# Performance work log

Measured on AMD Instinct MI355X. Metric: run time of the kernel, lower is better.

Reference implementation:

```python
import jax, jax.numpy as jnp
import numpy as np

BLOCK_K = 128  # per_1x128 block quantization: block_n=1 (per row), block_k=128


def _dequant(wq, scale):
    # wq: [E, N, K] quantized codes; scale: [E, N, ceil(K/BLOCK_K)]
    K = wq.shape[-1]
    s_full = jnp.repeat(scale, BLOCK_K, axis=-1)[..., :K]
    return wq * s_full


def setup_inputs() -> dict:
    key = jax.random.key(0)
    ks = jax.random.split(key, 6)
    T, E, H, I = 1024, 8, 1024, 768
    x = jax.random.normal(ks[0], (T, H), dtype=jnp.float32)
    router_logits = jax.random.normal(ks[1], (T, E), dtype=jnp.float32)
    # fp8 codes simulated as float values; block scales positive (scale_inv)
    w13_weight = jax.random.normal(ks[2], (E, 2 * I, H), dtype=jnp.float32) * 0.05
    w13_weight_scale_inv = jax.random.uniform(ks[3], (E, 2 * I, H // BLOCK_K), dtype=jnp.float32, minval=0.5, maxval=1.5)
    w2_weight = jax.random.normal(ks[4], (E, H, I), dtype=jnp.float32) * 0.05
    w2_weight_scale_inv = jax.random.uniform(ks[5], (E, H, I // BLOCK_K), dtype=jnp.float32, minval=0.5, maxval=1.5)
    return {
        "x": x,
        "router_logits": router_logits,
        "w13_weight": w13_weight,
        "w13_weight_scale_inv": w13_weight_scale_inv,
        "w2_weight": w2_weight,
        "w2_weight_scale_inv": w2_weight_scale_inv,
        "top_k": 2,
    }


def reference(x, router_logits, w13_weight, w13_weight_scale_inv, w2_weight, w2_weight_scale_inv, top_k):
    T, H = x.shape
    E = router_logits.shape[-1]
    I = w2_weight.shape[-1]

    # ---- dequantize block-scaled weights (inline dequant of fp8 grouped GEMM) ----
    w13 = _dequant(w13_weight, w13_weight_scale_inv)   # [E, 2I, H]
    w2 = _dequant(w2_weight, w2_weight_scale_inv)      # [E, H, I]

    # ---- routing: softmax scoring, top_k, renormalize ----
    probs = jax.nn.softmax(router_logits, axis=-1)     # [T, E]
    topk_w, topk_idx = jax.lax.top_k(probs, top_k)     # [T, K]
    topk_w = topk_w / jnp.sum(topk_w, axis=-1, keepdims=True)  # renormalize=True
    # dense combine weights [T, E] (scatter of top_k routing weights)
    combine = jnp.zeros((T, E), x.dtype).at[jnp.arange(T)[:, None], topk_idx].add(topk_w)

    # ---- grouped expert FFN (dense-over-experts reference) ----
    gate_up = jnp.einsum('th,enh->ten', x, w13)        # [T, E, 2I]
    gate, up = gate_up[..., :I], gate_up[..., I:]
    act = jax.nn.silu(gate) * up                       # silu activation ('silu')
    out_e = jnp.einsum('tei,ehi->teh', act, w2)        # [T, E, H]

    # ---- combine ----
    return jnp.einsum('teh,te->th', out_e, combine)    # [T, H]
```

## Files before the change

### kernel.cpp

```cpp
#include <hip/hip_runtime.h>

#define T_TOK 1024
#define H_DIM 1024
#define I_DIM 768
#define E_NUM 8

#define G13 1572864
#define G2   786432
#define GX   131072
#define PREP_BLOCKS 10240

typedef __bf16 bf16x8 __attribute__((ext_vector_type(8)));
typedef float  f32x4  __attribute__((ext_vector_type(4)));

__device__ inline bf16x8 cvt8(float4 a, float4 b, float s) {
    bf16x8 o;
    o[0] = (__bf16)(a.x * s); o[1] = (__bf16)(a.y * s);
    o[2] = (__bf16)(a.z * s); o[3] = (__bf16)(a.w * s);
    o[4] = (__bf16)(b.x * s); o[5] = (__bf16)(b.y * s);
    o[6] = (__bf16)(b.z * s); o[7] = (__bf16)(b.w * s);
    return o;
}

__global__ __launch_bounds__(256) void prep_kernel(
    const float* __restrict__ w13, const float* __restrict__ w13s,
    const float* __restrict__ w2,  const float* __restrict__ w2s,
    const float* __restrict__ x,   float4* __restrict__ out4,
    __bf16* __restrict__ w13d, __bf16* __restrict__ w2d, __bf16* __restrict__ xbf,
    const float* __restrict__ logits,
    int* __restrict__ counts, int* __restrict__ base,
    int* __restrict__ tok_list, float* __restrict__ wt_list)
{
    if (blockIdx.x == PREP_BLOCKS) {
        __shared__ int cnt[E_NUM];
        const int t0 = threadIdx.x;
        if (t0 < E_NUM) cnt[t0] = 0;
        __syncthreads();
#pragma unroll
        for (int tt = 0; tt < 4; tt++) {
            int t = t0 + tt * 256;
            float l[E_NUM];
#pragma unroll
            for (int e = 0; e < E_NUM; e++) l[e] = logits[t * E_NUM + e];
            int e0 = 0; float m0 = l[0];
#pragma unroll
            for (int e = 1; e < E_NUM; e++) if (l[e] > m0) { m0 = l[e]; e0 = e; }
            int e1 = -1; float m1 = -3e38f;
#pragma unroll
            for (int e = 0; e < E_NUM; e++) if (e != e0 && l[e] > m1) { m1 = l[e]; e1 = e; }
            float w0 = 1.0f / (1.0f + expf(m1 - m0));
            float w1 = 1.0f - w0;
            int p0 = atomicAdd(&cnt[e0], 1);
            tok_list[e0 * T_TOK + p0] = t;
            wt_list[e0 * T_TOK + p0] = w0;
            int p1 = atomicAdd(&cnt[e1], 1);
            tok_list[e1 * T_TOK + p1] = t;
            wt_list[e1 * T_TOK + p1] = w1;
        }
        __syncthreads();
        if (t0 == 0) {
            int s = 0;
            for (int e = 0; e < E_NUM; e++) { base[e] = s; counts[e] = cnt[e]; s += cnt[e]; }
        }
        return;
    }

    int g = blockIdx.x * 256 + threadIdx.x;
    if (g < G13) {
        int k8 = g & 127;
        int row = g >> 7;
        float s = w13s[(row << 3) | (k8 >> 4)];
        const float4* src = (const float4*)w13 + (size_t)g * 2;
        *(bf16x8*)(w13d + (size_t)g * 8) = cvt8(src[0], src[1], s);
    } else if (g < G13 + G2) {
        int g2 = g - G13;
        unsigned row = (unsigned)g2 / 96u;
        int k8 = g2 - row * 96;
        float s = w2s[row * 6 + (k8 >> 4)];
        const float4* src = (const float4*)w2 + (size_t)g2 * 2;
        *(bf16x8*)(w2d + (size_t)g2 * 8) = cvt8(src[0], src[1], s);
    } else if (g < G13 + G2 + GX) {
        int gx = g - (G13 + G2);
        const float4* src = (const float4*)x + (size_t)gx * 2;
        *(bf16x8*)(xbf + (size_t)gx * 8) = cvt8(src[0], src[1], 1.0f);
    } else {
        int go = g - (G13 + G2 + GX);
        float4 z = make_float4(0.f, 0.f, 0.f, 0.f);
        out4[2 * go] = z; out4[2 * go + 1] = z;
    }
}

#define MFMA(A, B, C) __builtin_amdgcn_mfma_f32_16x16x32_bf16(A, B, C, 0, 0, 0)

struct Stage { uint4 a0, a1, b0, b1, b2, b3; };

__device__ inline Stage ld_stage(const __bf16* pA0, const __bf16* pA1,
                                 const __bf16* pB, int k) {
    Stage s;
    s.a0 = *(const uint4*)(pA0 + k);
    s.a1 = *(const uint4*)(pA1 + k);
    s.b0 = *(const uint4*)(pB + k);
    s.b1 = *(const uint4*)(pB + k + 8);
    s.b2 = *(const uint4*)(pB + k + 16);
    s.b3 = *(const uint4*)(pB + k + 24);
    return s;
}

__device__ inline void st_stage(char* As, char* Bs, int aw0, int aw1,
                                int bw0, int bw1, int bw2, int bw3,
                                const Stage& s) {
    *(uint4*)(As + aw0) = s.a0;
    *(uint4*)(As + aw1) = s.a1;
    *(uint4*)(Bs + bw0) = s.b0;
    *(uint4*)(Bs + bw1) = s.b1;
    *(uint4*)(Bs + bw2) = s.b2;
    *(uint4*)(Bs + bw3) = s.b3;
}

__global__ __launch_bounds__(256, 3) void gemm1_kernel(
    const __bf16* __restrict__ xbf,
    const __bf16* __restrict__ w13d,
    const int* __restrict__ counts,
    const int* __restrict__ base,
    const int* __restrict__ tok_list,
    __bf16* __restrict__ act)
{
    const int bx = blockIdx.x;
    const int xcd = bx & 7, t = bx >> 3;
    const int p = t % 12, m = t / 12;
    const int P = xcd + 8 * p;
    const int nb = P % 12, e = P / 12;
    const int count = counts[e];
    const int m0 = m * 64;
    if (m0 >= count) return;
    const int n0 = nb * 64;
    const int abase = base[e];

    __shared__ union {
        struct { __bf16 Bs[2][128 * 64]; __bf16 As[2][64 * 64]; } s;
        float gu[64 * 132];
    } u;
    __shared__ int tokS[64];

    const int tid = threadIdx.x;
    if (tid < 64) {
        int r = m0 + tid;
        tokS[tid] = (r < count) ? tok_list[e * T_TOK + r] : tok_list[e * T_TOK];
    }
    __syncthreads();

    const int arow = tid >> 3, ag = tid & 7;
    const __bf16* pA0 = xbf + (size_t)tokS[arow] * H_DIM + ag * 8;
    const __bf16* pA1 = xbf + (size_t)tokS[arow + 32] * H_DIM + ag * 8;
    const int aw0 = arow * 128 + ((ag ^ (arow & 7)) << 4);
    const int aw1 = aw0 + 32 * 128;
    const int brow = tid >> 1, bg0 = (tid & 1) * 4;
    const int nB = (brow < 64) ? (n0 + brow) : (I_DIM + n0 + brow - 64);
    const __bf16* pB = w13d + ((size_t)e * 2 * I_DIM + nB) * H_DIM + bg0 * 8;
    const int bw0 = brow * 128 + (((bg0 + 0) ^ (brow & 7)) << 4);
    const int bw1 = brow * 128 + (((bg0 + 1) ^ (brow & 7)) << 4);
    const int bw2 = brow * 128 + (((bg0 + 2) ^ (brow & 7)) << 4);
    const int bw3 = brow * 128 + (((bg0 + 3) ^ (brow & 7)) << 4);

    const int wid = tid >> 6, lane = tid & 63, lrow = lane & 15, quad = lane >> 4;
    int aoff[2][4], boff[2][2];
#pragma unroll
    for (int kk = 0; kk < 2; kk++) {
        int gph = ((kk * 4 + quad) ^ (lrow & 7)) << 4;
#pragma unroll
        for (int i = 0; i < 4; i++) aoff[kk][i] = (i * 16 + lrow) * 128 + gph;
#pragma unroll
        for (int j = 0; j < 2; j++) boff[kk][j] = (wid * 32 + j * 16 + lrow) * 128 + gph;
    }

    f32x4 acc[4][2];
#pragma unroll
    for (int i = 0; i < 4; i++)
#pragma unroll
        for (int j = 0; j < 2; j++) { f32x4 z = {0.f, 0.f, 0.f, 0.f}; acc[i][j] = z; }

    char* A0 = (char*)u.s.As[0]; char* A1 = (char*)u.s.As[1];
    char* B0 = (char*)u.s.Bs[0]; char* B1 = (char*)u.s.Bs[1];

    auto compute = [&](const char* Ab, const char* Bb) {
#pragma unroll
        for (int kk = 0; kk < 2; kk++) {
            bf16x8 b0 = *(const bf16x8*)(Bb + boff[kk][0]);
            bf16x8 b1 = *(const bf16x8*)(Bb + boff[kk][1]);
#pragma unroll
            for (int i = 0; i < 4; i++) {
                bf16x8 a = *(const bf16x8*)(Ab + aoff[kk][i]);
                acc[i][0] = MFMA(a, b0, acc[i][0]);
                acc[i][1] = MFMA(a, b1, acc[i][1]);
            }
        }
    };

    Stage X = ld_stage(pA0, pA1, pB, 0);
    Stage Y = ld_stage(pA0, pA1, pB, 64);
    st_stage(A0, B0, aw0, aw1, bw0, bw1, bw2, bw3, X);
    X = ld_stage(pA0, pA1, pB, 2 * 64);
    __syncthreads();

#pragma unroll
    for (int uu = 0; uu < 8; ++uu) {
        st_stage(A1, B1, aw0, aw1, bw0, bw1, bw2, bw3, Y);
        if (2 * uu + 3 < 16) Y = ld_stage(pA0, pA1, pB, (2 * uu + 3) * 64);
        compute(A0, B0);
        __syncthreads();
        if (uu < 7) st_stage(A0, B0, aw0, aw1, bw0, bw1, bw2, bw3, X);
        if (2 * uu + 4 < 16) X = ld_stage(pA0, pA1, pB, (2 * uu + 4) * 64);
        compute(A1, B1);
        __syncthreads();
    }

#pragma unroll
    for (int i = 0; i < 4; i++)
#pragma unroll
        for (int j = 0; j < 2; j++)
#pragma unroll
            for (int r = 0; r < 4; r++) {
                int mr = i * 16 + quad * 4 + r;
                int c = wid * 32 + j * 16 + lrow;
                u.gu[mr * 132 + c] = acc[i][j][r];
            }
    __syncthreads();

#pragma unroll
    for (int ii = 0; ii < 16; ii++) {
        int o = ii * 256 + tid;
        int mr = o >> 6, c = o & 63;
        if (m0 + mr < count) {
            float g  = u.gu[mr * 132 + c];
            float up = u.gu[mr * 132 + 64 + c];
            float a  = g / (1.0f + expf(-g)) * up;
            act[(size_t)(abase + m0 + mr) * I_DIM + n0 + c] = (__bf16)a;
        }
    }
}

__global__ __launch_bounds__(256, 3) void gemm2_kernel(
    const __bf16* __restrict__ act,
    const __bf16* __restrict__ w2d,
    const int* __restrict__ counts,
    const int* __restrict__ base,
    const int* __restrict__ tok_list,
    const float* __restrict__ wt_list,
    float* __restrict__ out)
{
    const int bx = blockIdx.x;
    const int xcd = bx & 7, t = bx >> 3;
    const int p = t & 7, m = t >> 3;
    const int P = xcd + 8 * p;
    const int nb = P & 7, e = P >> 3;
    const int count = counts[e];
    const int m0 = m * 64;
    if (m0 >= count) return;
    const int n0 = nb * 128;
    const int abase = base[e];

    __shared__ struct { __bf16 Bs[2][128 * 64]; __bf16 As[2][64 * 64]; } s;

    const int tid = threadIdx.x;
    const int arow = tid >> 3, ag = tid & 7;
    int gr0 = abase + m0 + arow;      if (gr0 > 2 * T_TOK - 1) gr0 = 2 * T_TOK - 1;
    int gr1 = abase + m0 + arow + 32; if (gr1 > 2 * T_TOK - 1) gr1 = 2 * T_TOK - 1;
    const __bf16* pA0 = act + (size_t)gr0 * I_DIM + ag * 8;
    const __bf16* pA1 = act + (size_t)gr1 * I_DIM + ag * 8;
    const int aw0 = arow * 128 + ((ag ^ (arow & 7)) << 4);
    const int aw1 = aw0 + 32 * 128;

    const int brow = tid >> 1, bg0 = (tid & 1) * 4;
    const __bf16* pB = w2d + ((size_t)e * H_DIM + n0 + brow) * I_DIM + bg0 * 8;
    const int bw0 = brow * 128 + (((bg0 + 0) ^ (brow & 7)) << 4);
    const int bw1 = brow * 128 + (((bg0 + 1) ^ (brow & 7)) << 4);
    const int bw2 = brow * 128 + (((bg0 + 2) ^ (brow & 7)) << 4);
    const int bw3 = brow * 128 + (((bg0 + 3) ^ (brow & 7)) << 4);

    const int wid = tid >> 6, lane = tid & 63, lrow = lane & 15, quad = lane >> 4;
    int aoff[2][4], boff[2][2];
#pragma unroll
    for (int kk = 0; kk < 2; kk++) {
        int gph = ((kk * 4 + quad) ^ (lrow & 7)) << 4;
#pragma unroll
        for (int i = 0; i < 4; i++) aoff[kk][i] = (i * 16 + lrow) * 128 + gph;
#pragma unroll
        for (int j = 0; j < 2; j++) boff[kk][j] = (wid * 32 + j * 16 + lrow) * 128 + gph;
    }

    f32x4 acc[4][2];
#pragma unroll
    for (int i = 0; i < 4; i++)
#pragma unroll
        for (int j = 0; j < 2; j++) { f32x4 z = {0.f, 0.f, 0.f, 0.f}; acc[i][j] = z; }

    char* A0 = (char*)s.As[0]; char* A1 = (char*)s.As[1];
    char* B0 = (char*)s.Bs[0]; char* B1 = (char*)s.Bs[1];

    auto compute = [&](const char* Ab, const char* Bb) {
#pragma unroll
        for (int kk = 0; kk < 2; kk++) {
            bf16x8 b0 = *(const bf16x8*)(Bb + boff[kk][0]);
            bf16x8 b1 = *(const bf16x8*)(Bb + boff[kk][1]);
#pragma unroll
            for (int i = 0; i < 4; i++) {
                bf16x8 a = *(const bf16x8*)(Ab + aoff[kk][i]);
                acc[i][0] = MFMA(a, b0, acc[i][0]);
                acc[i][1] = MFMA(a, b1, acc[i][1]);
            }
        }
    };

    Stage X = ld_stage(pA0, pA1, pB, 0);
    Stage Y = ld_stage(pA0, pA1, pB, 64);
    st_stage(A0, B0, aw0, aw1, bw0, bw1, bw2, bw3, X);
    X = ld_stage(pA0, pA1, pB, 2 * 64);
    __syncthreads();

#pragma unroll
    for (int uu = 0; uu < 6; ++uu) {
        st_stage(A1, B1, aw0, aw1, bw0, bw1, bw2, bw3, Y);
        if (2 * uu + 3 < 12) Y = ld_stage(pA0, pA1, pB, (2 * uu + 3) * 64);
        compute(A0, B0);
        __syncthreads();
        if (uu < 5) st_stage(A0, B0, aw0, aw1, bw0, bw1, bw2, bw3, X);
        if (2 * uu + 4 < 12) X = ld_stage(pA0, pA1, pB, (2 * uu + 4) * 64);
        compute(A1, B1);
        __syncthreads();
    }

#pragma unroll
    for (int i = 0; i < 4; i++)
#pragma unroll
        for (int r = 0; r < 4; r++) {
            int mr = i * 16 + quad * 4 + r;
            if (m0 + mr < count) {
                int   tk = tok_list[e * T_TOK + m0 + mr];
                float w  = wt_list[e * T_TOK + m0 + mr];
#pragma unroll
                for (int j = 0; j < 2; j++) {
                    int h = n0 + wid * 32 + j * 16 + lrow;
                    atomicAdd(&out[(size_t)tk * H_DIM + h], w * acc[i][j][r]);
                }
            }
        }
}

extern "C" void kernel_launch(void* const* d_in, const int* in_sizes, int n_in,
                              void* d_out, int out_size, void* d_ws, size_t ws_size,
                              hipStream_t stream) {
    (void)in_sizes; (void)n_in; (void)out_size; (void)ws_size;
    const float* x      = (const float*)d_in[0];
    const float* logits = (const float*)d_in[1];
    const float* w13    = (const float*)d_in[2];
    const float* w13s   = (const float*)d_in[3];
    const float* w2     = (const float*)d_in[4];
    const float* w2s    = (const float*)d_in[5];
    float* out = (float*)d_out;

    char* ws = (char*)d_ws;
    int*    counts   = (int*)ws;
    int*    base     = (int*)(ws + 128);
    int*    tok_list = (int*)(ws + 256);
    float*  wt_list  = (float*)(ws + 256 + 32768);
    __bf16* act      = (__bf16*)(ws + 65792);
    __bf16* xbf      = (__bf16*)(ws + 65792 + 3145728);
    __bf16* w13d     = (__bf16*)(ws + 65792 + 3145728 + 2097152);
    __bf16* w2d      = (__bf16*)(ws + 65792 + 3145728 + 2097152 + 25165824);

    prep_kernel<<<dim3(PREP_BLOCKS + 1), 256, 0, stream>>>(
        w13, w13s, w2, w2s, x, (float4*)out, w13d, w2d, xbf,
        logits, counts, base, tok_list, wt_list);
    gemm1_kernel<<<dim3(1536), 256, 0, stream>>>(
        xbf, w13d, counts, base, tok_list, act);
    gemm2_kernel<<<dim3(1024), 256, 0, stream>>>(
        act, w2d, counts, base, tok_list, wt_list, out);
}
```

Before: 154.3 us.

## Fuse block-scale weight dequantization into GEMM B-tile loads

Drops the separate prep pass that converted all fp32 expert weights to scaled bf16 copies in workspace. Each GEMM kernel now loads the fp32 weights directly, applies the per-128 block scale held in registers, and converts to bf16 before writing to shared memory. Block-to-tile mapping is also changed so that consecutive blocks sweep token tiles of the same expert/N tile, which should improve cache reuse of the fp32 weights. The trade-off is twice the global bytes per B-tile load per block, repeated for each token tile, plus more registers and conversion work inside the GEMM loop.

```diff
diff --git a/kernel.cpp b/kernel.cpp
--- a/kernel.cpp
+++ b/kernel.cpp
@@ -5,10 +5,9 @@
 #define I_DIM 768
 #define E_NUM 8
 
-#define G13 1572864
-#define G2   786432
 #define GX   131072
-#define PREP_BLOCKS 10240
+#define GZ   131072
+#define PREP_BLOCKS 1024
 
 typedef __bf16 bf16x8 __attribute__((ext_vector_type(8)));
 typedef float  f32x4  __attribute__((ext_vector_type(4)));
@@ -22,11 +21,13 @@
     return o;
 }
 
+__device__ inline uint4 asu4(bf16x8 v) {
+    union { bf16x8 b; uint4 u; } c; c.b = v; return c.u;
+}
+
 __global__ __launch_bounds__(256) void prep_kernel(
-    const float* __restrict__ w13, const float* __restrict__ w13s,
-    const float* __restrict__ w2,  const float* __restrict__ w2s,
     const float* __restrict__ x,   float4* __restrict__ out4,
-    __bf16* __restrict__ w13d, __bf16* __restrict__ w2d, __bf16* __restrict__ xbf,
+    __bf16* __restrict__ xbf,
     const float* __restrict__ logits,
     int* __restrict__ counts, int* __restrict__ base,
     int* __restrict__ tok_list, float* __restrict__ wt_list)
@@ -66,25 +67,11 @@
     }
 
     int g = blockIdx.x * 256 + threadIdx.x;
-    if (g < G13) {
-        int k8 = g & 127;
-        int row = g >> 7;
-        float s = w13s[(row << 3) | (k8 >> 4)];
-        const float4* src = (const float4*)w13 + (size_t)g * 2;
-        *(bf16x8*)(w13d + (size_t)g * 8) = cvt8(src[0], src[1], s);
-    } else if (g < G13 + G2) {
-        int g2 = g - G13;
-        unsigned row = (unsigned)g2 / 96u;
-        int k8 = g2 - row * 96;
-        float s = w2s[row * 6 + (k8 >> 4)];
-        const float4* src = (const float4*)w2 + (size_t)g2 * 2;
-        *(bf16x8*)(w2d + (size_t)g2 * 8) = cvt8(src[0], src[1], s);
-    } else if (g < G13 + G2 + GX) {
-        int gx = g - (G13 + G2);
-        const float4* src = (const float4*)x + (size_t)gx * 2;
-        *(bf16x8*)(xbf + (size_t)gx * 8) = cvt8(src[0], src[1], 1.0f);
+    if (g < GX) {
+        const float4* src = (const float4*)x + (size_t)g * 2;
+        *(bf16x8*)(xbf + (size_t)g * 8) = cvt8(src[0], src[1], 1.0f);
     } else {
-        int go = g - (G13 + G2 + GX);
+        int go = g - GX;
         float4 z = make_float4(0.f, 0.f, 0.f, 0.f);
         out4[2 * go] = z; out4[2 * go + 1] = z;
     }
@@ -95,15 +82,18 @@
 struct Stage { uint4 a0, a1, b0, b1, b2, b3; };
 
 __device__ inline Stage ld_stage(const __bf16* pA0, const __bf16* pA1,
-                                 const __bf16* pB, int k) {
-    Stage s;
-    s.a0 = *(const uint4*)(pA0 + k);
-    s.a1 = *(const uint4*)(pA1 + k);
-    s.b0 = *(const uint4*)(pB + k);
-    s.b1 = *(const uint4*)(pB + k + 8);
-    s.b2 = *(const uint4*)(pB + k + 16);
-    s.b3 = *(const uint4*)(pB + k + 24);
-    return s;
+                                 const float* pB, int k, float s) {
+    Stage st;
+    st.a0 = *(const uint4*)(pA0 + k);
+    st.a1 = *(const uint4*)(pA1 + k);
+    const float4* q = (const float4*)(pB + k);
+    float4 q0 = q[0], q1 = q[1], q2 = q[2], q3 = q[3];
+    float4 q4 = q[4], q5 = q[5], q6 = q[6], q7 = q[7];
+    st.b0 = asu4(cvt8(q0, q1, s));
+    st.b1 = asu4(cvt8(q2, q3, s));
+    st.b2 = asu4(cvt8(q4, q5, s));
+    st.b3 = asu4(cvt8(q6, q7, s));
+    return st;
 }
 
 __device__ inline void st_stage(char* As, char* Bs, int aw0, int aw1,
@@ -119,7 +109,8 @@
 
 __global__ __launch_bounds__(256, 3) void gemm1_kernel(
     const __bf16* __restrict__ xbf,
-    const __bf16* __restrict__ w13d,
+    const float* __restrict__ w13,
+    const float* __restrict__ w13s,
     const int* __restrict__ counts,
     const int* __restrict__ base,
     const int* __restrict__ tok_list,
@@ -127,7 +118,7 @@
 {
     const int bx = blockIdx.x;
     const int xcd = bx & 7, t = bx >> 3;
-    const int p = t % 12, m = t / 12;
+    const int m = t & 15, p = t >> 4;
     const int P = xcd + 8 * p;
     const int nb = P % 12, e = P / 12;
     const int count = counts[e];
@@ -156,11 +147,15 @@
     const int aw1 = aw0 + 32 * 128;
     const int brow = tid >> 1, bg0 = (tid & 1) * 4;
     const int nB = (brow < 64) ? (n0 + brow) : (I_DIM + n0 + brow - 64);
-    const __bf16* pB = w13d + ((size_t)e * 2 * I_DIM + nB) * H_DIM + bg0 * 8;
+    const size_t r13 = (size_t)e * 2 * I_DIM + nB;
+    const float* pB = w13 + r13 * H_DIM + bg0 * 8;
     const int bw0 = brow * 128 + (((bg0 + 0) ^ (brow & 7)) << 4);
     const int bw1 = brow * 128 + (((bg0 + 1) ^ (brow & 7)) << 4);
     const int bw2 = brow * 128 + (((bg0 + 2) ^ (brow & 7)) << 4);
     const int bw3 = brow * 128 + (((bg0 + 3) ^ (brow & 7)) << 4);
+    const float4* srow = (const float4*)(w13s + r13 * 8);
+    float4 scA = srow[0], scB = srow[1];
+    float sc[8] = {scA.x, scA.y, scA.z, scA.w, scB.x, scB.y, scB.z, scB.w};
 
     const int wid = tid >> 6, lane = tid & 63, lrow = lane & 15, quad = lane >> 4;
     int aoff[2][4], boff[2][2];
@@ -196,20 +191,20 @@
         }
     };
 
-    Stage X = ld_stage(pA0, pA1, pB, 0);
-    Stage Y = ld_stage(pA0, pA1, pB, 64);
+    Stage X = ld_stage(pA0, pA1, pB, 0, sc[0]);
+    Stage Y = ld_stage(pA0, pA1, pB, 64, sc[0]);
     st_stage(A0, B0, aw0, aw1, bw0, bw1, bw2, bw3, X);
-    X = ld_stage(pA0, pA1, pB, 2 * 64);
+    X = ld_stage(pA0, pA1, pB, 2 * 64, sc[1]);
     __syncthreads();
 
 #pragma unroll
     for (int uu = 0; uu < 8; ++uu) {
         st_stage(A1, B1, aw0, aw1, bw0, bw1, bw2, bw3, Y);
-        if (2 * uu + 3 < 16) Y = ld_stage(pA0, pA1, pB, (2 * uu + 3) * 64);
+        if (2 * uu + 3 < 16) Y = ld_stage(pA0, pA1, pB, (2 * uu + 3) * 64, sc[uu + 1]);
         compute(A0, B0);
         __syncthreads();
         if (uu < 7) st_stage(A0, B0, aw0, aw1, bw0, bw1, bw2, bw3, X);
-        if (2 * uu + 4 < 16) X = ld_stage(pA0, pA1, pB, (2 * uu + 4) * 64);
+        if (2 * uu + 4 < 16) X = ld_stage(pA0, pA1, pB, (2 * uu + 4) * 64, sc[uu + 2]);
         compute(A1, B1);
         __syncthreads();
     }
@@ -241,7 +236,8 @@
 
 __global__ __launch_bounds__(256, 3) void gemm2_kernel(
     const __bf16* __restrict__ act,
-    const __bf16* __restrict__ w2d,
+    const float* __restrict__ w2,
+    const float* __restrict__ w2s,
     const int* __restrict__ counts,
     const int* __restrict__ base,
     const int* __restrict__ tok_list,
@@ -250,7 +246,7 @@
 {
     const int bx = blockIdx.x;
     const int xcd = bx & 7, t = bx >> 3;
-    const int p = t & 7, m = t >> 3;
+    const int m = t & 15, p = t >> 4;
     const int P = xcd + 8 * p;
     const int nb = P & 7, e = P >> 3;
     const int count = counts[e];
@@ -271,11 +267,16 @@
     const int aw1 = aw0 + 32 * 128;
 
     const int brow = tid >> 1, bg0 = (tid & 1) * 4;
-    const __bf16* pB = w2d + ((size_t)e * H_DIM + n0 + brow) * I_DIM + bg0 * 8;
+    const size_t r2 = (size_t)e * H_DIM + n0 + brow;
+    const float* pB = w2 + r2 * I_DIM + bg0 * 8;
     const int bw0 = brow * 128 + (((bg0 + 0) ^ (brow & 7)) << 4);
     const int bw1 = brow * 128 + (((bg0 + 1) ^ (brow & 7)) << 4);
     const int bw2 = brow * 128 + (((bg0 + 2) ^ (brow & 7)) << 4);
     const int bw3 = brow * 128 + (((bg0 + 3) ^ (brow & 7)) << 4);
+    const float* srow = w2s + r2 * 6;
+    float sc[6];
+#pragma unroll
+    for (int i = 0; i < 6; i++) sc[i] = srow[i];
 
     const int wid = tid >> 6, lane = tid & 63, lrow = lane & 15, quad = lane >> 4;
     int aoff[2][4], boff[2][2];
@@ -311,20 +312,20 @@
         }
     };
 
-    Stage X = ld_stage(pA0, pA1, pB, 0);
-    Stage Y = ld_stage(pA0, pA1, pB, 64);
+    Stage X = ld_stage(pA0, pA1, pB, 0, sc[0]);
+    Stage Y = ld_stage(pA0, pA1, pB, 64, sc[0]);
     st_stage(A0, B0, aw0, aw1, bw0, bw1, bw2, bw3, X);
-    X = ld_stage(pA0, pA1, pB, 2 * 64);
+    X = ld_stage(pA0, pA1, pB, 2 * 64, sc[1]);
     __syncthreads();
 
 #pragma unroll
     for (int uu = 0; uu < 6; ++uu) {
         st_stage(A1, B1, aw0, aw1, bw0, bw1, bw2, bw3, Y);
-        if (2 * uu + 3 < 12) Y = ld_stage(pA0, pA1, pB, (2 * uu + 3) * 64);
+        if (2 * uu + 3 < 12) Y = ld_stage(pA0, pA1, pB, (2 * uu + 3) * 64, sc[uu + 1]);
         compute(A0, B0);
         __syncthreads();
         if (uu < 5) st_stage(A0, B0, aw0, aw1, bw0, bw1, bw2, bw3, X);
-        if (2 * uu + 4 < 12) X = ld_stage(pA0, pA1, pB, (2 * uu + 4) * 64);
+        if (2 * uu + 4 < 12) X = ld_stage(pA0, pA1, pB, (2 * uu + 4) * 64, sc[uu + 2]);
         compute(A1, B1);
         __syncthreads();
     }
@@ -365,14 +366,11 @@
     float*  wt_list  = (float*)(ws + 256 + 32768);
     __bf16* act      = (__bf16*)(ws + 65792);
     __bf16* xbf      = (__bf16*)(ws + 65792 + 3145728);
-    __bf16* w13d     = (__bf16*)(ws + 65792 + 3145728 + 2097152);
-    __bf16* w2d      = (__bf16*)(ws + 65792 + 3145728 + 2097152 + 25165824);
 
     prep_kernel<<<dim3(PREP_BLOCKS + 1), 256, 0, stream>>>(
-        w13, w13s, w2, w2s, x, (float4*)out, w13d, w2d, xbf,
-        logits, counts, base, tok_list, wt_list);
+        x, (float4*)out, xbf, logits, counts, base, tok_list, wt_list);
     gemm1_kernel<<<dim3(1536), 256, 0, stream>>>(
-        xbf, w13d, counts, base, tok_list, act);
+        xbf, w13, w13s, counts, base, tok_list, act);
     gemm2_kernel<<<dim3(1024), 256, 0, stream>>>(
-        act, w2d, counts, base, tok_list, wt_list, out);
-}
+        act, w2, w2s, counts, base, tok_list, wt_list, out);
+}
```

Measured after the change: 230.0 us. 49.0% more time.

## Move w2 dequant into gemm1 launch and halve GEMM M-tile to 32 rows

Applied to the files above, without the earlier changes.

The w2 weight dequantization moves out of the prep kernel and into extra blocks of the gemm1 launch, so it can run alongside the first grouped GEMM instead of ahead of it. Both GEMM kernels switch from 64-row to 32-row token tiles, with grids sized for 32 possible tiles per expert. The smaller tile means more blocks and less padding waste on uneven expert loads. In exchange, each block reuses every B-tile load across half as many rows, so weight traffic per FLOP doubles, and the dequant blocks compete with the GEMM blocks for bandwidth.

```diff
diff --git a/kernel.cpp b/kernel.cpp
--- a/kernel.cpp
+++ b/kernel.cpp
@@ -5,10 +5,14 @@
 #define I_DIM 768
 #define E_NUM 8
 
+#define A_W13 6144
+#define A_X   512
+#define A_Z   512
 #define G13 1572864
 #define G2   786432
-#define GX   131072
-#define PREP_BLOCKS 10240
+
+#define GEMM1_BLOCKS 3072
+#define W2DQ_BLOCKS  3072
 
 typedef __bf16 bf16x8 __attribute__((ext_vector_type(8)));
 typedef float  f32x4  __attribute__((ext_vector_type(4)));
@@ -22,83 +26,75 @@
     return o;
 }
 
-__global__ __launch_bounds__(256) void prep_kernel(
+__global__ __launch_bounds__(256) void prep13_kernel(
     const float* __restrict__ w13, const float* __restrict__ w13s,
-    const float* __restrict__ w2,  const float* __restrict__ w2s,
     const float* __restrict__ x,   float4* __restrict__ out4,
-    __bf16* __restrict__ w13d, __bf16* __restrict__ w2d, __bf16* __restrict__ xbf,
+    __bf16* __restrict__ w13d,     __bf16* __restrict__ xbf,
     const float* __restrict__ logits,
     int* __restrict__ counts, int* __restrict__ base,
     int* __restrict__ tok_list, float* __restrict__ wt_list)
 {
-    if (blockIdx.x == PREP_BLOCKS) {
-        __shared__ int cnt[E_NUM];
-        const int t0 = threadIdx.x;
-        if (t0 < E_NUM) cnt[t0] = 0;
-        __syncthreads();
-#pragma unroll
-        for (int tt = 0; tt < 4; tt++) {
-            int t = t0 + tt * 256;
-            float l[E_NUM];
-#pragma unroll
-            for (int e = 0; e < E_NUM; e++) l[e] = logits[t * E_NUM + e];
-            int e0 = 0; float m0 = l[0];
-#pragma unroll
-            for (int e = 1; e < E_NUM; e++) if (l[e] > m0) { m0 = l[e]; e0 = e; }
-            int e1 = -1; float m1 = -3e38f;
-#pragma unroll
-            for (int e = 0; e < E_NUM; e++) if (e != e0 && l[e] > m1) { m1 = l[e]; e1 = e; }
-            float w0 = 1.0f / (1.0f + expf(m1 - m0));
-            float w1 = 1.0f - w0;
-            int p0 = atomicAdd(&cnt[e0], 1);
-            tok_list[e0 * T_TOK + p0] = t;
-            wt_list[e0 * T_TOK + p0] = w0;
-            int p1 = atomicAdd(&cnt[e1], 1);
-            tok_list[e1 * T_TOK + p1] = t;
-            wt_list[e1 * T_TOK + p1] = w1;
-        }
-        __syncthreads();
-        if (t0 == 0) {
-            int s = 0;
-            for (int e = 0; e < E_NUM; e++) { base[e] = s; counts[e] = cnt[e]; s += cnt[e]; }
-        }
-        return;
-    }
-
-    int g = blockIdx.x * 256 + threadIdx.x;
-    if (g < G13) {
+    const int bx = blockIdx.x;
+    if (bx < A_W13) {
+        int g = bx * 256 + threadIdx.x;
         int k8 = g & 127;
         int row = g >> 7;
         float s = w13s[(row << 3) | (k8 >> 4)];
         const float4* src = (const float4*)w13 + (size_t)g * 2;
         *(bf16x8*)(w13d + (size_t)g * 8) = cvt8(src[0], src[1], s);
-    } else if (g < G13 + G2) {
-        int g2 = g - G13;
-        unsigned row = (unsigned)g2 / 96u;
-        int k8 = g2 - row * 96;
-        float s = w2s[row * 6 + (k8 >> 4)];
-        const float4* src = (const float4*)w2 + (size_t)g2 * 2;
-        *(bf16x8*)(w2d + (size_t)g2 * 8) = cvt8(src[0], src[1], s);
-    } else if (g < G13 + G2 + GX) {
-        int gx = g - (G13 + G2);
-        const float4* src = (const float4*)x + (size_t)gx * 2;
-        *(bf16x8*)(xbf + (size_t)gx * 8) = cvt8(src[0], src[1], 1.0f);
-    } else {
-        int go = g - (G13 + G2 + GX);
+        return;
+    }
+    if (bx < A_W13 + A_X) {
+        int g = (bx - A_W13) * 256 + threadIdx.x;
+        const float4* src = (const float4*)x + (size_t)g * 2;
+        *(bf16x8*)(xbf + (size_t)g * 8) = cvt8(src[0], src[1], 1.0f);
+        return;
+    }
+    if (bx < A_W13 + A_X + A_Z) {
+        int go = (bx - A_W13 - A_X) * 256 + threadIdx.x;
         float4 z = make_float4(0.f, 0.f, 0.f, 0.f);
         out4[2 * go] = z; out4[2 * go + 1] = z;
+        return;
+    }
+    __shared__ int cnt[E_NUM];
+    const int t0 = threadIdx.x;
+    if (t0 < E_NUM) cnt[t0] = 0;
+    __syncthreads();
+#pragma unroll
+    for (int tt = 0; tt < 4; tt++) {
+        int t = t0 + tt * 256;
+        float l[E_NUM];
+#pragma unroll
+        for (int e = 0; e < E_NUM; e++) l[e] = logits[t * E_NUM + e];
+        int e0 = 0; float m0 = l[0];
+#pragma unroll
+        for (int e = 1; e < E_NUM; e++) if (l[e] > m0) { m0 = l[e]; e0 = e; }
+        int e1 = -1; float m1 = -3e38f;
+#pragma unroll
+        for (int e = 0; e < E_NUM; e++) if (e != e0 && l[e] > m1) { m1 = l[e]; e1 = e; }
+        float w0 = 1.0f / (1.0f + expf(m1 - m0));
+        float w1 = 1.0f - w0;
+        int p0 = atomicAdd(&cnt[e0], 1);
+        tok_list[e0 * T_TOK + p0] = t;
+        wt_list[e0 * T_TOK + p0] = w0;
+        int p1 = atomicAdd(&cnt[e1], 1);
+        tok_list[e1 * T_TOK + p1] = t;
+        wt_list[e1 * T_TOK + p1] = w1;
+    }
+    __syncthreads();
+    if (t0 == 0) {
+        int s = 0;
+        for (int e = 0; e < E_NUM; e++) { base[e] = s; counts[e] = cnt[e]; s += cnt[e]; }
     }
 }
 
 #define MFMA(A, B, C) __builtin_amdgcn_mfma_f32_16x16x32_bf16(A, B, C, 0, 0, 0)
 
-struct Stage { uint4 a0, a1, b0, b1, b2, b3; };
-
-__device__ inline Stage ld_stage(const __bf16* pA0, const __bf16* pA1,
-                                 const __bf16* pB, int k) {
+struct Stage { uint4 a0, b0, b1, b2, b3; };
+
+__device__ inline Stage ld_stage(const __bf16* pA0, const __bf16* pB, int k) {
     Stage s;
     s.a0 = *(const uint4*)(pA0 + k);
-    s.a1 = *(const uint4*)(pA1 + k);
     s.b0 = *(const uint4*)(pB + k);
     s.b1 = *(const uint4*)(pB + k + 8);
     s.b2 = *(const uint4*)(pB + k + 16);
@@ -106,11 +102,10 @@
     return s;
 }
 
-__device__ inline void st_stage(char* As, char* Bs, int aw0, int aw1,
+__device__ inline void st_stage(char* As, char* Bs, int aw0,
                                 int bw0, int bw1, int bw2, int bw3,
                                 const Stage& s) {
     *(uint4*)(As + aw0) = s.a0;
-    *(uint4*)(As + aw1) = s.a1;
     *(uint4*)(Bs + bw0) = s.b0;
     *(uint4*)(Bs + bw1) = s.b1;
     *(uint4*)(Bs + bw2) = s.b2;
@@ -123,27 +118,40 @@
     const int* __restrict__ counts,
     const int* __restrict__ base,
     const int* __restrict__ tok_list,
-    __bf16* __restrict__ act)
+    __bf16* __restrict__ act,
+    const float* __restrict__ w2,
+    const float* __restrict__ w2s,
+    __bf16* __restrict__ w2d)
 {
     const int bx = blockIdx.x;
+    if (bx >= GEMM1_BLOCKS) {
+        int g2 = (bx - GEMM1_BLOCKS) * 256 + threadIdx.x;
+        unsigned row = (unsigned)g2 / 96u;
+        int k8 = g2 - row * 96;
+        float s = w2s[row * 6 + (k8 >> 4)];
+        const float4* src = (const float4*)w2 + (size_t)g2 * 2;
+        *(bf16x8*)(w2d + (size_t)g2 * 8) = cvt8(src[0], src[1], s);
+        return;
+    }
+
     const int xcd = bx & 7, t = bx >> 3;
-    const int p = t % 12, m = t / 12;
+    const int m = t & 31, p = t >> 5;
     const int P = xcd + 8 * p;
     const int nb = P % 12, e = P / 12;
     const int count = counts[e];
-    const int m0 = m * 64;
+    const int m0 = m * 32;
     if (m0 >= count) return;
     const int n0 = nb * 64;
     const int abase = base[e];
 
     __shared__ union {
-        struct { __bf16 Bs[2][128 * 64]; __bf16 As[2][64 * 64]; } s;
-        float gu[64 * 132];
+        struct { __bf16 Bs[2][128 * 64]; __bf16 As[2][32 * 64]; } s;
+        float gu[32 * 132];
     } u;
-    __shared__ int tokS[64];
+    __shared__ int tokS[32];
 
     const int tid = threadIdx.x;
-    if (tid < 64) {
+    if (tid < 32) {
         int r = m0 + tid;
         tokS[tid] = (r < count) ? tok_list[e * T_TOK + r] : tok_list[e * T_TOK];
     }
@@ -151,9 +159,7 @@
 
     const int arow = tid >> 3, ag = tid & 7;
     const __bf16* pA0 = xbf + (size_t)tokS[arow] * H_DIM + ag * 8;
-    const __bf16* pA1 = xbf + (size_t)tokS[arow + 32] * H_DIM + ag * 8;
     const int aw0 = arow * 128 + ((ag ^ (arow & 7)) << 4);
-    const int aw1 = aw0 + 32 * 128;
     const int brow = tid >> 1, bg0 = (tid & 1) * 4;
     const int nB = (brow < 64) ? (n0 + brow) : (I_DIM + n0 + brow - 64);
     const __bf16* pB = w13d + ((size_t)e * 2 * I_DIM + nB) * H_DIM + bg0 * 8;
@@ -163,19 +169,19 @@
     const int bw3 = brow * 128 + (((bg0 + 3) ^ (brow & 7)) << 4);
 
     const int wid = tid >> 6, lane = tid & 63, lrow = lane & 15, quad = lane >> 4;
-    int aoff[2][4], boff[2][2];
+    int aoff[2][2], boff[2][2];
 #pragma unroll
     for (int kk = 0; kk < 2; kk++) {
         int gph = ((kk * 4 + quad) ^ (lrow & 7)) << 4;
 #pragma unroll
-        for (int i = 0; i < 4; i++) aoff[kk][i] = (i * 16 + lrow) * 128 + gph;
+        for (int i = 0; i < 2; i++) aoff[kk][i] = (i * 16 + lrow) * 128 + gph;
 #pragma unroll
         for (int j = 0; j < 2; j++) boff[kk][j] = (wid * 32 + j * 16 + lrow) * 128 + gph;
     }
 
-    f32x4 acc[4][2];
-#pragma unroll
-    for (int i = 0; i < 4; i++)
+    f32x4 acc[2][2];
+#pragma unroll
+    for (int i = 0; i < 2; i++)
 #pragma unroll
         for (int j = 0; j < 2; j++) { f32x4 z = {0.f, 0.f, 0.f, 0.f}; acc[i][j] = z; }
 
@@ -188,7 +194,7 @@
             bf16x8 b0 = *(const bf16x8*)(Bb + boff[kk][0]);
             bf16x8 b1 = *(const bf16x8*)(Bb + boff[kk][1]);
 #pragma unroll
-            for (int i = 0; i < 4; i++) {
+            for (int i = 0; i < 2; i++) {
                 bf16x8 a = *(const bf16x8*)(Ab + aoff[kk][i]);
                 acc[i][0] = MFMA(a, b0, acc[i][0]);
                 acc[i][1] = MFMA(a, b1, acc[i][1]);
@@ -196,26 +202,26 @@
         }
     };
 
-    Stage X = ld_stage(pA0, pA1, pB, 0);
-    Stage Y = ld_stage(pA0, pA1, pB, 64);
-    st_stage(A0, B0, aw0, aw1, bw0, bw1, bw2, bw3, X);
-    X = ld_stage(pA0, pA1, pB, 2 * 64);
+    Stage X = ld_stage(pA0, pB, 0);
+    Stage Y = ld_stage(pA0, pB, 64);
+    st_stage(A0, B0, aw0, bw0, bw1, bw2, bw3, X);
+    X = ld_stage(pA0, pB, 2 * 64);
     __syncthreads();
 
 #pragma unroll
     for (int uu = 0; uu < 8; ++uu) {
-        st_stage(A1, B1, aw0, aw1, bw0, bw1, bw2, bw3, Y);
-        if (2 * uu + 3 < 16) Y = ld_stage(pA0, pA1, pB, (2 * uu + 3) * 64);
+        st_stage(A1, B1, aw0, bw0, bw1, bw2, bw3, Y);
+        if (2 * uu + 3 < 16) Y = ld_stage(pA0, pB, (2 * uu + 3) * 64);
         compute(A0, B0);
         __syncthreads();
-        if (uu < 7) st_stage(A0, B0, aw0, aw1, bw0, bw1, bw2, bw3, X);
-        if (2 * uu + 4 < 16) X = ld_stage(pA0, pA1, pB, (2 * uu + 4) * 64);
+        if (uu < 7) st_stage(A0, B0, aw0, bw0, bw1, bw2, bw3, X);
+        if (2 * uu + 4 < 16) X = ld_stage(pA0, pB, (2 * uu + 4) * 64);
         compute(A1, B1);
         __syncthreads();
     }
 
 #pragma unroll
-    for (int i = 0; i < 4; i++)
+    for (int i = 0; i < 2; i++)
 #pragma unroll
         for (int j = 0; j < 2; j++)
 #pragma unroll
@@ -227,7 +233,7 @@
     __syncthreads();
 
 #pragma unroll
-    for (int ii = 0; ii < 16; ii++) {
+    for (int ii = 0; ii < 8; ii++) {
         int o = ii * 256 + tid;
         int mr = o >> 6, c = o & 63;
         if (m0 + mr < count) {
@@ -250,25 +256,22 @@
 {
     const int bx = blockIdx.x;
     const int xcd = bx & 7, t = bx >> 3;
-    const int p = t & 7, m = t >> 3;
+    const int m = t & 31, p = t >> 5;
     const int P = xcd + 8 * p;
     const int nb = P & 7, e = P >> 3;
     const int count = counts[e];
-    const int m0 = m * 64;
+    const int m0 = m * 32;
     if (m0 >= count) return;
     const int n0 = nb * 128;
     const int abase = base[e];
 
-    __shared__ struct { __bf16 Bs[2][128 * 64]; __bf16 As[2][64 * 64]; } s;
+    __shared__ struct { __bf16 Bs[2][128 * 64]; __bf16 As[2][32 * 64]; } s;
 
     const int tid = threadIdx.x;
     const int arow = tid >> 3, ag = tid & 7;
     int gr0 = abase + m0 + arow;      if (gr0 > 2 * T_TOK - 1) gr0 = 2 * T_TOK - 1;
-    int gr1 = abase + m0 + arow + 32; if (gr1 > 2 * T_TOK - 1) gr1 = 2 * T_TOK - 1;
     const __bf16* pA0 = act + (size_t)gr0 * I_DIM + ag * 8;
-    const __bf16* pA1 = act + (size_t)gr1 * I_DIM + ag * 8;
     const int aw0 = arow * 128 + ((ag ^ (arow & 7)) << 4);
-    const int aw1 = aw0 + 32 * 128;
 
     const int brow = tid >> 1, bg0 = (tid & 1) * 4;
     const __bf16* pB = w2d + ((size_t)e * H_DIM + n0 + brow) * I_DIM + bg0 * 8;
@@ -278,19 +281,19 @@
     const int bw3 = brow * 128 + (((bg0 + 3) ^ (brow & 7)) << 4);
 
     const int wid = tid >> 6, lane = tid & 63, lrow = lane & 15, quad = lane >> 4;
-    int aoff[2][4], boff[2][2];
+    int aoff[2][2], boff[2][2];
 #pragma unroll
     for (int kk = 0; kk < 2; kk++) {
         int gph = ((kk * 4 + quad) ^ (lrow & 7)) << 4;
 #pragma unroll
-        for (int i = 0; i < 4; i++) aoff[kk][i] = (i * 16 + lrow) * 128 + gph;
+        for (int i = 0; i < 2; i++) aoff[kk][i] = (i * 16 + lrow) * 128 + gph;
 #pragma unroll
         for (int j = 0; j < 2; j++) boff[kk][j] = (wid * 32 + j * 16 + lrow) * 128 + gph;
     }
 
-    f32x4 acc[4][2];
-#pragma unroll
-    for (int i = 0; i < 4; i++)
+    f32x4 acc[2][2];
+#pragma unroll
+    for (int i = 0; i < 2; i++)
 #pragma unroll
         for (int j = 0; j < 2; j++) { f32x4 z = {0.f, 0.f, 0.f, 0.f}; acc[i][j] = z; }
 
@@ -303,7 +306,7 @@
             bf16x8 b0 = *(const bf16x8*)(Bb + boff[kk][0]);
             bf16x8 b1 = *(const bf16x8*)(Bb + boff[kk][1]);
 #pragma unroll
-            for (int i = 0; i < 4; i++) {
+            for (int i = 0; i < 2; i++) {
                 bf16x8 a = *(const bf16x8*)(Ab + aoff[kk][i]);
                 acc[i][0] = MFMA(a, b0, acc[i][0]);
                 acc[i][1] = MFMA(a, b1, acc[i][1]);
@@ -311,26 +314,26 @@
         }
     };
 
-    Stage X = ld_stage(pA0, pA1, pB, 0);
-    Stage Y = ld_stage(pA0, pA1, pB, 64);
-    st_stage(A0, B0, aw0, aw1, bw0, bw1, bw2, bw3, X);
-    X = ld_stage(pA0, pA1, pB, 2 * 64);
+    Stage X = ld_stage(pA0, pB, 0);
+    Stage Y = ld_stage(pA0, pB, 64);
+    st_stage(A0, B0, aw0, bw0, bw1, bw2, bw3, X);
+    X = ld_stage(pA0, pB, 2 * 64);
     __syncthreads();
 
 #pragma unroll
     for (int uu = 0; uu < 6; ++uu) {
-        st_stage(A1, B1, aw0, aw1, bw0, bw1, bw2, bw3, Y);
-        if (2 * uu + 3 < 12) Y = ld_stage(pA0, pA1, pB, (2 * uu + 3) * 64);
+        st_stage(A1, B1, aw0, bw0, bw1, bw2, bw3, Y);
+        if (2 * uu + 3 < 12) Y = ld_stage(pA0, pB, (2 * uu + 3) * 64);
         compute(A0, B0);
         __syncthreads();
-        if (uu < 5) st_stage(A0, B0, aw0, aw1, bw0, bw1, bw2, bw3, X);
-        if (2 * uu + 4 < 12) X = ld_stage(pA0, pA1, pB, (2 * uu + 4) * 64);
+        if (uu < 5) st_stage(A0, B0, aw0, bw0, bw1, bw2, bw3, X);
+        if (2 * uu + 4 < 12) X = ld_stage(pA0, pB, (2 * uu + 4) * 64);
         compute(A1, B1);
         __syncthreads();
     }
 
 #pragma unroll
-    for (int i = 0; i < 4; i++)
+    for (int i = 0; i < 2; i++)
 #pragma unroll
         for (int r = 0; r < 4; r++) {
             int mr = i * 16 + quad * 4 + r;
@@ -368,11 +371,11 @@
     __bf16* w13d     = (__bf16*)(ws + 65792 + 3145728 + 2097152);
     __bf16* w2d      = (__bf16*)(ws + 65792 + 3145728 + 2097152 + 25165824);
 
-    prep_kernel<<<dim3(PREP_BLOCKS + 1), 256, 0, stream>>>(
-        w13, w13s, w2, w2s, x, (float4*)out, w13d, w2d, xbf,
+    prep13_kernel<<<dim3(A_W13 + A_X + A_Z + 1), 256, 0, stream>>>(
+        w13, w13s, x, (float4*)out, w13d, xbf,
         logits, counts, base, tok_list, wt_list);
-    gemm1_kernel<<<dim3(1536), 256, 0, stream>>>(
-        xbf, w13d, counts, base, tok_list, act);
-    gemm2_kernel<<<dim3(1024), 256, 0, stream>>>(
+    gemm1_kernel<<<dim3(GEMM1_BLOCKS + W2DQ_BLOCKS), 256, 0, stream>>>(
+        xbf, w13d, counts, base, tok_list, act, w2, w2s, w2d);
+    gemm2_kernel<<<dim3(2048), 256, 0, stream>>>(
         act, w2d, counts, base, tok_list, wt_list, out);
 }
```

Result: slower. 164.7 us (+6.7%).
